# Performance work log

Measured on AMD Instinct MI355X. Metric: run time of the kernel, lower is better.

Reference implementation:

```python
import jax, jax.numpy as jnp
import numpy as np

SEQ, BATCH, IN, HID = 2048, 64, 256, 256

def setup_inputs() -> dict:
    key = jax.random.key(0)
    k1, k2, k3, k4, k5 = jax.random.split(key, 5)
    s = 1.0 / np.sqrt(HID)  # torch RNN default init scale
    return {
        "input": jax.random.normal(k1, (SEQ, BATCH, IN), dtype=jnp.float32),
        "W_ih": jax.random.uniform(k2, (HID, IN), dtype=jnp.float32, minval=-s, maxval=s),
        "W_hh": jax.random.uniform(k3, (HID, HID), dtype=jnp.float32, minval=-s, maxval=s),
        "b_ih": jax.random.uniform(k4, (HID,), dtype=jnp.float32, minval=-s, maxval=s),
        "b_hh": jax.random.uniform(k5, (HID,), dtype=jnp.float32, minval=-s, maxval=s),
    }

def reference(input, W_ih, W_hh, b_ih, b_hh):
    # Precompute input projection for all timesteps: [S, B, H]
    x_proj = jnp.einsum('sbi,hi->sbh', input, W_ih) + b_ih + b_hh
    h0 = jnp.zeros((input.shape[1], W_hh.shape[0]), dtype=input.dtype)

    def step(h, xp):
        h_new = jnp.tanh(xp + h @ W_hh.T)
        return h_new, h_new

    _, outs = jax.lax.scan(step, h0, x_proj)  # outs: [S, B, H]
    return outs.reshape(-1, W_hh.shape[0])
```

## Files before the change

kernel.cpp:

```cpp
#include <hip/hip_runtime.h>
#include <stdint.h>

#define SEQ   2048
#define NBATCH 64
#define IND   256
#define HIDN  256

using short8  = __attribute__((ext_vector_type(8))) short;
using floatx4 = __attribute__((ext_vector_type(4))) float;

__device__ __forceinline__ unsigned bf16r(float f) {
    unsigned u = __builtin_bit_cast(unsigned, f);
    return (u + 0x8000u) >> 16;
}

__device__ __forceinline__ short8 pack8(floatx4 f0, floatx4 f1) {
    short8 s;
    s[0] = (short)bf16r(f0[0]); s[1] = (short)bf16r(f0[1]);
    s[2] = (short)bf16r(f0[2]); s[3] = (short)bf16r(f0[3]);
    s[4] = (short)bf16r(f1[0]); s[5] = (short)bf16r(f1[1]);
    s[6] = (short)bf16r(f1[2]); s[7] = (short)bf16r(f1[3]);
    return s;
}

__device__ __forceinline__ float tanh_fast(float z) {
    float a = __builtin_amdgcn_exp2f(z * 2.8853900817779268f);
    return __builtin_fmaf(-2.0f, __builtin_amdgcn_rcpf(1.0f + a), 1.0f);
}

__device__ __forceinline__ void lds_barrier() {
    __builtin_amdgcn_s_waitcnt(0xc07f);
    __builtin_amdgcn_s_barrier();
}

__global__ __launch_bounds__(256, 2) void proj_kernel(
    const float* __restrict__ inp, const float* __restrict__ W_ih,
    const float* __restrict__ b_ih, const float* __restrict__ b_hh,
    unsigned short* __restrict__ xp)
{
    const int tid  = threadIdx.x;
    const int w    = tid >> 6;
    const int lane = tid & 63;
    const int c    = lane & 15;
    const int q    = lane >> 4;
    const size_t R0 = (size_t)blockIdx.x * 64;

    short8 bfr[4][8];
    float bias[4];
    #pragma unroll
    for (int tn = 0; tn < 4; ++tn) {
        const int n = 64 * w + 16 * tn + c;
        bias[tn] = b_ih[n] + b_hh[n];
        #pragma unroll
        for (int kk = 0; kk < 8; ++kk) {
            const float* p = W_ih + (size_t)n * 256 + kk * 32 + q * 8;
            bfr[tn][kk] = pack8(*(const floatx4*)p, *(const floatx4*)(p + 4));
        }
    }

    #pragma unroll
    for (int mt = 0; mt < 4; ++mt) {
        short8 afr[8];
        const float* arow = inp + (R0 + 16 * mt + c) * 256;
        #pragma unroll
        for (int kk = 0; kk < 8; ++kk) {
            const float* p = arow + kk * 32 + q * 8;
            afr[kk] = pack8(*(const floatx4*)p, *(const floatx4*)(p + 4));
        }
        floatx4 acc[4];
        #pragma unroll
        for (int tn = 0; tn < 4; ++tn) {
            floatx4 a0; a0[0] = bias[tn]; a0[1] = bias[tn]; a0[2] = bias[tn]; a0[3] = bias[tn];
            acc[tn] = a0;
        }
        #pragma unroll
        for (int kk = 0; kk < 8; ++kk)
            #pragma unroll
            for (int tn = 0; tn < 4; ++tn)
                acc[tn] = __builtin_amdgcn_mfma_f32_16x16x32_bf16(afr[kk], bfr[tn][kk], acc[tn], 0, 0, 0);
        #pragma unroll
        for (int tn = 0; tn < 4; ++tn) {
            const unsigned col = 64 * w + 16 * tn + c;
            #pragma unroll
            for (int r = 0; r < 4; ++r) {
                const size_t row = R0 + 16 * mt + q * 4 + r;
                xp[row * 256 + col] = (unsigned short)bf16r(acc[tn][r]);
            }
        }
    }
}

__global__ __launch_bounds__(512, 2) void rnn_kernel(
    const float* __restrict__ W_hh,
    const unsigned short* __restrict__ xp,
    float* __restrict__ out)
{
    __shared__ __align__(16) unsigned short hbuf[2][16 * 264];
    const int tid  = threadIdx.x;
    const int w    = tid >> 6, lane = tid & 63;
    const int c    = lane & 15, q = lane >> 4;
    const int B0   = blockIdx.x * 16;

    short8 bfr[2][8];
    #pragma unroll
    for (int t2 = 0; t2 < 2; ++t2) {
        const int n = 32 * w + 16 * t2 + c;
        #pragma unroll
        for (int kk = 0; kk < 8; ++kk) {
            const float* p = W_hh + (size_t)n * 256 + kk * 32 + q * 8;
            bfr[t2][kk] = pack8(*(const floatx4*)p, *(const floatx4*)(p + 4));
        }
    }

    for (int i = tid; i < 2 * 16 * 264; i += 512) (&hbuf[0][0])[i] = 0;
    __syncthreads();

    const unsigned lofs = (unsigned)(B0 + q * 4) * 256 + 32 * w + c;
    const unsigned short* xq = xp + lofs;
    float* oq = out + lofs;

    unsigned xa[8], xb[8];
    #pragma unroll
    for (int i = 0; i < 8; ++i) {
        const int t2 = i & 1, r = i >> 1;
        xa[i] = xq[r * 256 + t2 * 16];
        xb[i] = xq[16384 + r * 256 + t2 * 16];
    }

    auto step = [&](int t, int sel, unsigned* xv) {
        short8 afr[8];
        #pragma unroll
        for (int kk = 0; kk < 8; ++kk)
            afr[kk] = *(const short8*)&hbuf[sel][c * 264 + kk * 32 + q * 8];

        floatx4 acc[2];
        #pragma unroll
        for (int t2 = 0; t2 < 2; ++t2) {
            floatx4 a0;
            a0[0] = __builtin_bit_cast(float, xv[0 * 2 + t2] << 16);
            a0[1] = __builtin_bit_cast(float, xv[1 * 2 + t2] << 16);
            a0[2] = __builtin_bit_cast(float, xv[2 * 2 + t2] << 16);
            a0[3] = __builtin_bit_cast(float, xv[3 * 2 + t2] << 16);
            acc[t2] = a0;
        }

        {
            const int tp = (t + 2 < SEQ) ? (t + 2) : (SEQ - 1);
            const unsigned short* p = xq + (size_t)tp * 16384;
            #pragma unroll
            for (int i = 0; i < 8; ++i) {
                const int t2 = i & 1, r = i >> 1;
                xv[i] = p[r * 256 + t2 * 16];
            }
        }

        #pragma unroll
        for (int kk = 0; kk < 8; ++kk)
            #pragma unroll
            for (int t2 = 0; t2 < 2; ++t2)
                acc[t2] = __builtin_amdgcn_mfma_f32_16x16x32_bf16(afr[kk], bfr[t2][kk], acc[t2], 0, 0, 0);

        float* op = oq + (size_t)t * 16384;
        unsigned short* hw = &hbuf[sel ^ 1][0];
        #pragma unroll
        for (int t2 = 0; t2 < 2; ++t2) {
            #pragma unroll
            for (int r = 0; r < 4; ++r) {
                const float hn = tanh_fast(acc[t2][r]);
                op[r * 256 + t2 * 16] = hn;
                hw[(q * 4 + r) * 264 + 32 * w + 16 * t2 + c] = (unsigned short)bf16r(hn);
            }
        }
        lds_barrier();
    };

    for (int t = 0; t < SEQ; t += 2) {
        step(t, 0, xa);
        step(t + 1, 1, xb);
    }
}

extern "C" void kernel_launch(void* const* d_in, const int* in_sizes, int n_in,
                              void* d_out, int out_size, void* d_ws, size_t ws_size,
                              hipStream_t stream) {
    const float* input = (const float*)d_in[0];
    const float* W_ih  = (const float*)d_in[1];
    const float* W_hh  = (const float*)d_in[2];
    const float* b_ih  = (const float*)d_in[3];
    const float* b_hh  = (const float*)d_in[4];
    float* out = (float*)d_out;
    unsigned short* xp = (unsigned short*)d_ws;

    proj_kernel<<<(SEQ * NBATCH) / 64, 256, 0, stream>>>(input, W_ih, b_ih, b_hh, xp);
    rnn_kernel<<<4, 512, 0, stream>>>(W_hh, xp, out);
}
```

Measured before the change: 1.658 ms.

## Transpose recurrent MFMA so outputs are contiguous, vectorize x loads and h stores

Swaps the MFMA operand order so W_hh is the A operand and h the B operand. Each lane then holds four consecutive hidden units for one batch row rather than four batch rows. This lets the per-step x_proj reads, output writes and LDS hidden-state writes use vector accesses (4x bf16, float4, packed 2x uint) instead of scalar strided ones. It also uses the hardware packed bf16 convert instruction, which rounds differently from the manual rounding used before. The intent is to cut memory and LDS instruction count on the serial recurrence's critical path.

```diff
diff --git a/kernel.cpp b/kernel.cpp
--- a/kernel.cpp
+++ b/kernel.cpp
@@ -8,6 +8,8 @@
 
 using short8  = __attribute__((ext_vector_type(8))) short;
 using floatx4 = __attribute__((ext_vector_type(4))) float;
+using us4     = __attribute__((ext_vector_type(4))) unsigned short;
+using uintx2  = __attribute__((ext_vector_type(2))) unsigned;
 
 __device__ __forceinline__ unsigned bf16r(float f) {
     unsigned u = __builtin_bit_cast(unsigned, f);
@@ -26,6 +28,12 @@
 __device__ __forceinline__ float tanh_fast(float z) {
     float a = __builtin_amdgcn_exp2f(z * 2.8853900817779268f);
     return __builtin_fmaf(-2.0f, __builtin_amdgcn_rcpf(1.0f + a), 1.0f);
+}
+
+__device__ __forceinline__ unsigned cvt_pk_bf16(float lo, float hi) {
+    unsigned r;
+    asm("v_cvt_pk_bf16_f32 %0, %1, %2" : "=v"(r) : "v"(lo), "v"(hi));
+    return r;
 }
 
 __device__ __forceinline__ void lds_barrier() {
@@ -101,75 +109,76 @@
     const int c    = lane & 15, q = lane >> 4;
     const int B0   = blockIdx.x * 16;
 
-    short8 bfr[2][8];
+    short8 wfr[2][8];
     #pragma unroll
     for (int t2 = 0; t2 < 2; ++t2) {
         const int n = 32 * w + 16 * t2 + c;
         #pragma unroll
         for (int kk = 0; kk < 8; ++kk) {
             const float* p = W_hh + (size_t)n * 256 + kk * 32 + q * 8;
-            bfr[t2][kk] = pack8(*(const floatx4*)p, *(const floatx4*)(p + 4));
+            wfr[t2][kk] = pack8(*(const floatx4*)p, *(const floatx4*)(p + 4));
         }
     }
 
     for (int i = tid; i < 2 * 16 * 264; i += 512) (&hbuf[0][0])[i] = 0;
     __syncthreads();
 
-    const unsigned lofs = (unsigned)(B0 + q * 4) * 256 + 32 * w + c;
+    const unsigned lofs = (unsigned)(B0 + c) * 256 + 32 * w + 4 * q;
     const unsigned short* xq = xp + lofs;
     float* oq = out + lofs;
-
-    unsigned xa[8], xb[8];
-    #pragma unroll
-    for (int i = 0; i < 8; ++i) {
-        const int t2 = i & 1, r = i >> 1;
-        xa[i] = xq[r * 256 + t2 * 16];
-        xb[i] = xq[16384 + r * 256 + t2 * 16];
-    }
-
-    auto step = [&](int t, int sel, unsigned* xv) {
-        short8 afr[8];
+    const unsigned wofs = (unsigned)c * 264 + 32 * w + 4 * q;
+
+    us4 xa[2], xb[2];
+    #pragma unroll
+    for (int t2 = 0; t2 < 2; ++t2) {
+        xa[t2] = *(const us4*)(xq + 16 * t2);
+        xb[t2] = *(const us4*)(xq + 16384 + 16 * t2);
+    }
+
+    auto step = [&](int t, int sel, us4* xv) {
+        short8 hfr[8];
         #pragma unroll
         for (int kk = 0; kk < 8; ++kk)
-            afr[kk] = *(const short8*)&hbuf[sel][c * 264 + kk * 32 + q * 8];
+            hfr[kk] = *(const short8*)&hbuf[sel][c * 264 + kk * 32 + q * 8];
 
         floatx4 acc[2];
         #pragma unroll
         for (int t2 = 0; t2 < 2; ++t2) {
             floatx4 a0;
-            a0[0] = __builtin_bit_cast(float, xv[0 * 2 + t2] << 16);
-            a0[1] = __builtin_bit_cast(float, xv[1 * 2 + t2] << 16);
-            a0[2] = __builtin_bit_cast(float, xv[2 * 2 + t2] << 16);
-            a0[3] = __builtin_bit_cast(float, xv[3 * 2 + t2] << 16);
+            a0[0] = __builtin_bit_cast(float, (unsigned)xv[t2][0] << 16);
+            a0[1] = __builtin_bit_cast(float, (unsigned)xv[t2][1] << 16);
+            a0[2] = __builtin_bit_cast(float, (unsigned)xv[t2][2] << 16);
+            a0[3] = __builtin_bit_cast(float, (unsigned)xv[t2][3] << 16);
             acc[t2] = a0;
         }
 
         {
             const int tp = (t + 2 < SEQ) ? (t + 2) : (SEQ - 1);
             const unsigned short* p = xq + (size_t)tp * 16384;
-            #pragma unroll
-            for (int i = 0; i < 8; ++i) {
-                const int t2 = i & 1, r = i >> 1;
-                xv[i] = p[r * 256 + t2 * 16];
-            }
+            xv[0] = *(const us4*)(p);
+            xv[1] = *(const us4*)(p + 16);
         }
 
         #pragma unroll
         for (int kk = 0; kk < 8; ++kk)
             #pragma unroll
             for (int t2 = 0; t2 < 2; ++t2)
-                acc[t2] = __builtin_amdgcn_mfma_f32_16x16x32_bf16(afr[kk], bfr[t2][kk], acc[t2], 0, 0, 0);
+                acc[t2] = __builtin_amdgcn_mfma_f32_16x16x32_bf16(wfr[t2][kk], hfr[kk], acc[t2], 0, 0, 0);
 
         float* op = oq + (size_t)t * 16384;
         unsigned short* hw = &hbuf[sel ^ 1][0];
         #pragma unroll
         for (int t2 = 0; t2 < 2; ++t2) {
-            #pragma unroll
-            for (int r = 0; r < 4; ++r) {
-                const float hn = tanh_fast(acc[t2][r]);
-                op[r * 256 + t2 * 16] = hn;
-                hw[(q * 4 + r) * 264 + 32 * w + 16 * t2 + c] = (unsigned short)bf16r(hn);
-            }
+            const float h0 = tanh_fast(acc[t2][0]);
+            const float h1 = tanh_fast(acc[t2][1]);
+            const float h2 = tanh_fast(acc[t2][2]);
+            const float h3 = tanh_fast(acc[t2][3]);
+            floatx4 o; o[0] = h0; o[1] = h1; o[2] = h2; o[3] = h3;
+            *reinterpret_cast<floatx4*>(op + 16 * t2) = o;
+            uintx2 hv;
+            hv[0] = cvt_pk_bf16(h0, h1);
+            hv[1] = cvt_pk_bf16(h2, h3);
+            *reinterpret_cast<uintx2*>(hw + wofs + 16 * t2) = hv;
         }
         lds_barrier();
     };
```

Result: slower. 1.955 ms (+17.9%).
